# Performance work log

Hardware: AMD Instinct MI355X
Metric: run time of the kernel (lower is better)

## Reference

```python
import jax, jax.numpy as jnp
import numpy as np

N_SPANS = 4096
EMB_DIM = 384
HEADS = 4
DECAY_LAMBDA = 5.0
THRESHOLD = 0.1
NEG_SLOPE = 0.2  # PyG GATConv default leaky_relu slope


def setup_inputs() -> dict:
    key = jax.random.key(0)
    k1, k2, k3, k4, k5, k6 = jax.random.split(key, 6)
    embeddings = jax.random.normal(k1, (N_SPANS, EMB_DIM), dtype=jnp.float32)
    span_positions = jnp.sort(
        jax.random.randint(k2, (N_SPANS, 2), 0, 100000), axis=1
    ).astype(jnp.int64)
    # GATConv params: lin (no bias), per-head attention vectors, output bias
    glorot = 1.0 / np.sqrt(EMB_DIM)
    W = jax.random.normal(k3, (EMB_DIM, HEADS, EMB_DIM), dtype=jnp.float32) * glorot
    att_src = jax.random.normal(k4, (HEADS, EMB_DIM), dtype=jnp.float32) * glorot
    att_dst = jax.random.normal(k5, (HEADS, EMB_DIM), dtype=jnp.float32) * glorot
    bias = jnp.zeros((EMB_DIM,), dtype=jnp.float32)
    return {
        "embeddings": embeddings,
        "span_positions": span_positions,
        "W": W,
        "att_src": att_src,
        "att_dst": att_dst,
        "bias": bias,
    }


def _adjacency_mask(embeddings):
    # A_ij = cos_sim(e_i, e_j) * exp(-|i - j| / lambda); edges where A > 0.1
    n = embeddings.shape[0]
    en = embeddings / jnp.linalg.norm(embeddings, axis=1, keepdims=True)
    cos_sim = en @ en.T  # [N, N]
    idx = jnp.arange(n, dtype=embeddings.dtype)
    decay = jnp.exp(-jnp.abs(idx[None, :] - idx[:, None]) / DECAY_LAMBDA)
    adj = cos_sim * decay
    # diagonal is 1.0 > threshold, so self-loops (required by GATConv) are present
    return adj > THRESHOLD  # symmetric mask: mask[i, j] == edge j -> i


def reference(embeddings, span_positions, W, att_src, att_dst, bias):
    mask = _adjacency_mask(embeddings)  # [N_dst, N_src]
    # GATConv(heads=4, concat=False): project, per-head additive attention
    x = jnp.einsum("nd,dhe->nhe", embeddings, W)  # [N, H, E]
    a_src = jnp.einsum("nhe,he->nh", x, att_src)  # [N, H]
    a_dst = jnp.einsum("nhe,he->nh", x, att_dst)  # [N, H]
    # logits[i, j, h] for edge j -> i
    logits = jax.nn.leaky_relu(a_dst[:, None, :] + a_src[None, :, :], NEG_SLOPE)
    logits = jnp.where(mask[:, :, None], logits, jnp.float32(-jnp.inf))
    alpha = jax.nn.softmax(logits, axis=1)  # softmax over incoming sources j
    out = jnp.einsum("ijh,jhe->ihe", alpha, x)  # [N, H, E]
    out = out.mean(axis=1) + bias  # concat=False -> mean over heads, then bias
    return out
```

## Files before the change

kernel.cpp:

```cpp
#include <hip/hip_runtime.h>
#include <hip/hip_bf16.h>
#include <math.h>

#define N_SPANS 4096
#define EMB 384
#define HEADS 4
#define HE (HEADS * EMB)
#define BAND 11
#define BW (2 * BAND + 1)

typedef short bf16x8 __attribute__((ext_vector_type(8)));
typedef float f32x4 __attribute__((ext_vector_type(4)));

__device__ __forceinline__ unsigned short f2bf(float f) {
    union { float f; unsigned u; } x; x.f = f;
    unsigned r = x.u + 0x7fffu + ((x.u >> 16) & 1u);
    return (unsigned short)(r >> 16);
}
__device__ __forceinline__ float bf2f(unsigned short u) {
    union { unsigned u; float f; } x; x.u = ((unsigned)u) << 16; return x.f;
}

__device__ __forceinline__ float wave_sum(float v) {
    #pragma unroll
    for (int off = 32; off; off >>= 1) v += __shfl_xor(v, off, 64);
    return v;
}
__device__ __forceinline__ float wave_max(float v) {
    #pragma unroll
    for (int off = 32; off; off >>= 1) v = fmaxf(v, __shfl_xor(v, off, 64));
    return v;
}

__device__ __forceinline__ void gl2lds16(const void* g, void* l) {
    __builtin_amdgcn_global_load_lds(
        (const __attribute__((address_space(1))) void*)(uintptr_t)g,
        (__attribute__((address_space(3))) void*)(unsigned)(uintptr_t)l,
        16, 0, 0);
}

__global__ __launch_bounds__(256) void prep(const float* __restrict__ E,
                                            const float* __restrict__ W,
                                            unsigned short* __restrict__ Ebf,
                                            unsigned short* __restrict__ Wt,
                                            float* __restrict__ invn,
                                            float* __restrict__ Dots,
                                            float* __restrict__ attacc) {
    __shared__ float tile[32][33];
    const int b = blockIdx.x;
    const int tid = threadIdx.x;
    if (b < 1024) {
        const int lane = tid & 63, w = tid >> 6;
        const int n = b * 4 + w;
        const float4* er4 = (const float4*)(E + (size_t)n * EMB);
        const int dmax = (n >= N_SPANS - BAND) ? (N_SPANS - 1 - n) : BAND;
        const float4* nb4[BAND];
        #pragma unroll
        for (int d = 1; d <= BAND; ++d) {
            int j = n + d; if (j > N_SPANS - 1) j = N_SPANS - 1;
            nb4[d - 1] = (const float4*)(E + (size_t)j * EMB);
        }
        float acc[12];
        #pragma unroll
        for (int d = 0; d < 12; ++d) acc[d] = 0.f;
        #pragma unroll
        for (int mq = 0; mq < 2; ++mq) {
            const int idx = mq * 64 + lane;
            if (idx < 96) {
                float4 v = er4[idx];
                acc[0] += v.x * v.x + v.y * v.y + v.z * v.z + v.w * v.w;
                ushort4 pb;
                pb.x = f2bf(v.x); pb.y = f2bf(v.y); pb.z = f2bf(v.z); pb.w = f2bf(v.w);
                ((ushort4*)(Ebf + (size_t)n * EMB))[idx] = pb;
                #pragma unroll
                for (int d = 1; d <= BAND; ++d) {
                    float4 u = nb4[d - 1][idx];
                    float dd = v.x * u.x + v.y * u.y + v.z * u.z + v.w * u.w;
                    acc[d] += (d <= dmax) ? dd : 0.f;
                }
            }
        }
        #pragma unroll
        for (int d = 0; d < 12; ++d) acc[d] = wave_sum(acc[d]);
        float dval = 0.f;
        #pragma unroll
        for (int d = 1; d <= BAND; ++d) if (lane == d) dval = acc[d];
        if (lane >= 1 && lane <= BAND) Dots[(size_t)n * 12 + lane] = dval;
        if (lane == 0) invn[n] = 1.0f / sqrtf(acc[0]);
    } else if (b < 1600) {
        const int t = b - 1024;
        const int n0 = (t % 48) * 32;
        const int k0 = (t / 48) * 32;
        const int tx = tid & 31, ty = tid >> 5;
        #pragma unroll
        for (int q = 0; q < 4; ++q)
            tile[ty + q * 8][tx] = W[(k0 + ty + q * 8) * HE + n0 + tx];
        __syncthreads();
        #pragma unroll
        for (int q = 0; q < 4; ++q)
            Wt[(n0 + ty + q * 8) * EMB + k0 + tx] = f2bf(tile[tx][ty + q * 8]);
    } else {
        const int t = b - 1600;
        ((float4*)attacc)[t * 256 + tid] = make_float4(0.f, 0.f, 0.f, 0.f);
    }
}

__global__ __launch_bounds__(256) void gemm_attn(const unsigned short* __restrict__ Ebf,
                                                 const unsigned short* __restrict__ Wt,
                                                 const float* __restrict__ attS,
                                                 const float* __restrict__ attD,
                                                 unsigned short* __restrict__ Xb,
                                                 float* __restrict__ asrc,
                                                 float* __restrict__ adst) {
    __shared__ unsigned short As[128 * 32];
    __shared__ unsigned short Bs[128 * 32];
    const int tid = threadIdx.x;
    const int lane = tid & 63;
    const int wave = tid >> 6;
    const int m0 = blockIdx.y * 128;
    const int n0 = blockIdx.x * 128;
    const int wr = (wave >> 1) * 64;
    const int wc = (wave & 1) * 64;
    const int quad = lane >> 4;
    const int l16 = lane & 15;

    const int schunk = (lane & 3) ^ ((lane >> 3) & 3);
    const char* Ab = (const char*)Ebf + (size_t)(m0 + wave * 32 + (lane >> 2)) * 768 + schunk * 16;
    const char* Bb = (const char*)Wt  + (size_t)(n0 + wave * 32 + (lane >> 2)) * 768 + schunk * 16;
    char* AsB = (char*)As + wave * 32 * 64;
    char* BsB = (char*)Bs + wave * 32 * 64;

    const int rchunk = (quad ^ ((l16 >> 1) & 3)) * 16;

    f32x4 acc[4][4];
    #pragma unroll
    for (int i = 0; i < 4; ++i)
        #pragma unroll
        for (int j = 0; j < 4; ++j) acc[i][j] = 0.f;

    for (int kt = 0; kt < 12; ++kt) {
        const int kb = kt * 64;
        __syncthreads();
        gl2lds16(Ab + kb,            AsB);
        gl2lds16(Ab + kb + 16 * 768, AsB + 16 * 64);
        gl2lds16(Bb + kb,            BsB);
        gl2lds16(Bb + kb + 16 * 768, BsB + 16 * 64);
        __syncthreads();

        bf16x8 af[4], bfr[4];
        #pragma unroll
        for (int t = 0; t < 4; ++t) {
            af[t]  = *(const bf16x8*)((const char*)As + (wr + t * 16 + l16) * 64 + rchunk);
            bfr[t] = *(const bf16x8*)((const char*)Bs + (wc + t * 16 + l16) * 64 + rchunk);
        }
        #pragma unroll
        for (int ti = 0; ti < 4; ++ti)
            #pragma unroll
            for (int tj = 0; tj < 4; ++tj)
                acc[ti][tj] = __builtin_amdgcn_mfma_f32_16x16x32_bf16(
                    af[ti], bfr[tj], acc[ti][tj], 0, 0, 0);
    }

    const int hblk = (n0 + wc) / EMB;
    float aS[4], aD[4];
    #pragma unroll
    for (int tj = 0; tj < 4; ++tj) {
        int col = n0 + wc + tj * 16 + l16;
        aS[tj] = attS[col];
        aD[tj] = attD[col];
    }
    #pragma unroll
    for (int ti = 0; ti < 4; ++ti)
        #pragma unroll
        for (int r = 0; r < 4; ++r) {
            float ps = 0.f, pd = 0.f;
            #pragma unroll
            for (int tj = 0; tj < 4; ++tj) {
                float v = acc[ti][tj][r];
                ps += v * aS[tj];
                pd += v * aD[tj];
            }
            #pragma unroll
            for (int off = 1; off < 16; off <<= 1) {
                ps += __shfl_xor(ps, off, 64);
                pd += __shfl_xor(pd, off, 64);
            }
            if (l16 == 0) {
                int row = m0 + wr + ti * 16 + quad * 4 + r;
                atomicAdd(&asrc[row * HEADS + hblk], ps);
                atomicAdd(&adst[row * HEADS + hblk], pd);
            }
        }

    #pragma unroll
    for (int ti = 0; ti < 4; ++ti)
        #pragma unroll
        for (int tj = 0; tj < 4; ++tj) {
            int col = n0 + wc + tj * 16 + l16;
            #pragma unroll
            for (int r = 0; r < 4; ++r) {
                int row = m0 + wr + ti * 16 + quad * 4 + r;
                Xb[row * HE + col] = f2bf(acc[ti][tj][r]);
            }
        }
}

__global__ __launch_bounds__(256) void band_attn(const float* __restrict__ invn,
                                                 const float* __restrict__ Dots,
                                                 const float* __restrict__ asrc,
                                                 const float* __restrict__ adst,
                                                 const unsigned short* __restrict__ Xb,
                                                 const float* __restrict__ bias,
                                                 float* __restrict__ out) {
    __shared__ float sAl[4][BW][4];
    __shared__ int sList[4][24];
    const int tid = threadIdx.x, lane = tid & 63, w = tid >> 6;
    const int i = blockIdx.x * 4 + w;
    const int jo = lane;
    const int j = i - BAND + jo;
    const bool inb = (jo < BW) && (j >= 0) && (j < N_SPANS);
    const int jc = inb ? j : i;

    float dotv = 0.f;
    if (inb) {
        if (jo < BAND)      dotv = Dots[(size_t)j * 12 + (BAND - jo)];
        else if (jo > BAND) dotv = Dots[(size_t)i * 12 + (jo - BAND)];
    }
    bool flag;
    if (jo == BAND) {
        flag = true;
    } else {
        int dd = jo < BAND ? BAND - jo : jo - BAND;
        float a = ((dotv * invn[i]) * invn[jc]) * expf(-(float)dd * 0.2f);
        flag = inb && (a > 0.1f);
    }

    unsigned long long mbits = __ballot(flag);
    const int cnt = __popcll(mbits);
    const int rank = __popcll(mbits & ((1ull << jo) - 1ull));
    if (flag) sList[w][rank] = jo;

    const float4 ad = ((const float4*)adst)[i];
    const float4 as = inb ? ((const float4*)asrc)[jc] : make_float4(0.f, 0.f, 0.f, 0.f);
    float al[4];
    #pragma unroll
    for (int h = 0; h < 4; ++h) {
        float z = (&ad.x)[h] + (&as.x)[h];
        z = (z >= 0.f) ? z : 0.2f * z;
        float lg = flag ? z : -INFINITY;
        float mx = wave_max(lg);
        float ex = flag ? expf(lg - mx) : 0.f;
        float sm = wave_sum(ex);
        al[h] = ex / sm;
    }
    if (flag) *(float4*)&sAl[w][jo][0] = make_float4(al[0], al[1], al[2], al[3]);

    #pragma unroll
    for (int mq = 0; mq < 2; ++mq) {
        const int e4 = mq * 64 + lane;
        if (e4 < 96) {
            float4 a = make_float4(0.f, 0.f, 0.f, 0.f);
            for (int ii = 0; ii < cnt; ++ii) {
                const int joL = sList[w][ii];
                const int jj = i - BAND + joL;
                const float4 a4 = *(const float4*)&sAl[w][joL][0];
                const ushort4* xr = (const ushort4*)(Xb + (size_t)jj * HE);
                ushort4 h0 = xr[e4], h1 = xr[e4 + 96], h2 = xr[e4 + 192], h3 = xr[e4 + 288];
                a.x += a4.x * bf2f(h0.x) + a4.y * bf2f(h1.x) + a4.z * bf2f(h2.x) + a4.w * bf2f(h3.x);
                a.y += a4.x * bf2f(h0.y) + a4.y * bf2f(h1.y) + a4.z * bf2f(h2.y) + a4.w * bf2f(h3.y);
                a.z += a4.x * bf2f(h0.z) + a4.y * bf2f(h1.z) + a4.z * bf2f(h2.z) + a4.w * bf2f(h3.z);
                a.w += a4.x * bf2f(h0.w) + a4.y * bf2f(h1.w) + a4.z * bf2f(h2.w) + a4.w * bf2f(h3.w);
            }
            const float4 bv = ((const float4*)bias)[e4];
            float4 o;
            o.x = 0.25f * a.x + bv.x;
            o.y = 0.25f * a.y + bv.y;
            o.z = 0.25f * a.z + bv.z;
            o.w = 0.25f * a.w + bv.w;
            ((float4*)(out + (size_t)i * EMB))[e4] = o;
        }
    }
}

extern "C" void kernel_launch(void* const* d_in, const int* in_sizes, int n_in,
                              void* d_out, int out_size, void* d_ws, size_t ws_size,
                              hipStream_t stream) {
    const float* E       = (const float*)d_in[0];
    const float* W       = (const float*)d_in[2];
    const float* att_src = (const float*)d_in[3];
    const float* att_dst = (const float*)d_in[4];
    const float* bias    = (const float*)d_in[5];
    float* out = (float*)d_out;

    char* ws = (char*)d_ws;
    unsigned short* Xb  = (unsigned short*)ws;
    unsigned short* Ebf = (unsigned short*)(ws + 12582912);
    unsigned short* Wt  = (unsigned short*)(ws + 15728640);
    float* invn         = (float*)(ws + 16908288);
    float* asrc         = (float*)(ws + 16924672);
    float* adst         = (float*)(ws + 16990208);
    float* Dots         = (float*)(ws + 17055744);

    prep<<<1632, 256, 0, stream>>>(E, W, Ebf, Wt, invn, Dots, asrc );
    gemm_attn<<<dim3(12, 32), 256, 0, stream>>>(Ebf, Wt, att_src, att_dst, Xb, asrc, adst);
    band_attn<<<1024, 256, 0, stream>>>(invn, Dots, asrc, adst, Xb, bias, out);
}
```

Baseline: 108.1 us.

## Double-buffer GEMM LDS tiles and halve N tile to 64 for more blocks

The projection GEMM now prefetches the next K-slice into a second LDS buffer while computing the current one, removing one barrier per iteration. The N tile shrinks from 128 to 64, doubling the grid from 384 to 768 blocks so the 256 CUs are better filled. The cost is more global reads of the A tile across blocks, fewer MFMAs per LDS load, and twice as many atomic adds for the attention scores.

```diff
diff --git a/kernel.cpp b/kernel.cpp
--- a/kernel.cpp
+++ b/kernel.cpp
@@ -112,60 +112,73 @@
                                                  unsigned short* __restrict__ Xb,
                                                  float* __restrict__ asrc,
                                                  float* __restrict__ adst) {
-    __shared__ unsigned short As[128 * 32];
-    __shared__ unsigned short Bs[128 * 32];
+    __shared__ unsigned short As[2 * 128 * 32];
+    __shared__ unsigned short Bs[2 * 64 * 32];
     const int tid = threadIdx.x;
     const int lane = tid & 63;
     const int wave = tid >> 6;
     const int m0 = blockIdx.y * 128;
-    const int n0 = blockIdx.x * 128;
-    const int wr = (wave >> 1) * 64;
-    const int wc = (wave & 1) * 64;
+    const int n0 = blockIdx.x * 64;
+    const int wrow = (wave >> 1) * 64;
+    const int wcol = (wave & 1) * 32;
     const int quad = lane >> 4;
     const int l16 = lane & 15;
 
     const int schunk = (lane & 3) ^ ((lane >> 3) & 3);
     const char* Ab = (const char*)Ebf + (size_t)(m0 + wave * 32 + (lane >> 2)) * 768 + schunk * 16;
-    const char* Bb = (const char*)Wt  + (size_t)(n0 + wave * 32 + (lane >> 2)) * 768 + schunk * 16;
-    char* AsB = (char*)As + wave * 32 * 64;
-    char* BsB = (char*)Bs + wave * 32 * 64;
+    const char* Bb = (const char*)Wt  + (size_t)(n0 + wave * 16 + (lane >> 2)) * 768 + schunk * 16;
+    char* AsW = (char*)As + wave * 2048;
+    char* BsW = (char*)Bs + wave * 1024;
 
     const int rchunk = (quad ^ ((l16 >> 1) & 3)) * 16;
 
-    f32x4 acc[4][4];
+    f32x4 acc[4][2];
     #pragma unroll
     for (int i = 0; i < 4; ++i)
         #pragma unroll
-        for (int j = 0; j < 4; ++j) acc[i][j] = 0.f;
-
+        for (int j = 0; j < 2; ++j) acc[i][j] = 0.f;
+
+    gl2lds16(Ab,            AsW);
+    gl2lds16(Ab + 16 * 768, AsW + 1024);
+    gl2lds16(Bb,            BsW);
+    __syncthreads();
+
+    int cur = 0;
     for (int kt = 0; kt < 12; ++kt) {
-        const int kb = kt * 64;
-        __syncthreads();
-        gl2lds16(Ab + kb,            AsB);
-        gl2lds16(Ab + kb + 16 * 768, AsB + 16 * 64);
-        gl2lds16(Bb + kb,            BsB);
-        gl2lds16(Bb + kb + 16 * 768, BsB + 16 * 64);
-        __syncthreads();
-
-        bf16x8 af[4], bfr[4];
-        #pragma unroll
-        for (int t = 0; t < 4; ++t) {
-            af[t]  = *(const bf16x8*)((const char*)As + (wr + t * 16 + l16) * 64 + rchunk);
-            bfr[t] = *(const bf16x8*)((const char*)Bs + (wc + t * 16 + l16) * 64 + rchunk);
-        }
+        if (kt < 11) {
+            const int kb = (kt + 1) * 64;
+            const int bufo = (cur ^ 1) * 8192;
+            const int bufoB = (cur ^ 1) * 4096;
+            gl2lds16(Ab + kb,            AsW + bufo);
+            gl2lds16(Ab + kb + 16 * 768, AsW + bufo + 1024);
+            gl2lds16(Bb + kb,            BsW + bufoB);
+        }
+
+        const char* aBase = (const char*)As + cur * 8192;
+        const char* bBase = (const char*)Bs + cur * 4096;
+        bf16x8 af[4], bfr[2];
+        #pragma unroll
+        for (int t = 0; t < 4; ++t)
+            af[t] = *(const bf16x8*)(aBase + (wrow + t * 16 + l16) * 64 + rchunk);
+        #pragma unroll
+        for (int t = 0; t < 2; ++t)
+            bfr[t] = *(const bf16x8*)(bBase + (wcol + t * 16 + l16) * 64 + rchunk);
         #pragma unroll
         for (int ti = 0; ti < 4; ++ti)
             #pragma unroll
-            for (int tj = 0; tj < 4; ++tj)
+            for (int tj = 0; tj < 2; ++tj)
                 acc[ti][tj] = __builtin_amdgcn_mfma_f32_16x16x32_bf16(
                     af[ti], bfr[tj], acc[ti][tj], 0, 0, 0);
-    }
-
-    const int hblk = (n0 + wc) / EMB;
-    float aS[4], aD[4];
-    #pragma unroll
-    for (int tj = 0; tj < 4; ++tj) {
-        int col = n0 + wc + tj * 16 + l16;
+
+        __syncthreads();
+        cur ^= 1;
+    }
+
+    const int hblk = (n0 + wcol) / EMB;
+    float aS[2], aD[2];
+    #pragma unroll
+    for (int tj = 0; tj < 2; ++tj) {
+        int col = n0 + wcol + tj * 16 + l16;
         aS[tj] = attS[col];
         aD[tj] = attD[col];
     }
@@ -175,7 +188,7 @@
         for (int r = 0; r < 4; ++r) {
             float ps = 0.f, pd = 0.f;
             #pragma unroll
-            for (int tj = 0; tj < 4; ++tj) {
+            for (int tj = 0; tj < 2; ++tj) {
                 float v = acc[ti][tj][r];
                 ps += v * aS[tj];
                 pd += v * aD[tj];
@@ -186,7 +199,7 @@
                 pd += __shfl_xor(pd, off, 64);
             }
             if (l16 == 0) {
-                int row = m0 + wr + ti * 16 + quad * 4 + r;
+                int row = m0 + wrow + ti * 16 + quad * 4 + r;
                 atomicAdd(&asrc[row * HEADS + hblk], ps);
                 atomicAdd(&adst[row * HEADS + hblk], pd);
             }
@@ -195,11 +208,11 @@
     #pragma unroll
     for (int ti = 0; ti < 4; ++ti)
         #pragma unroll
-        for (int tj = 0; tj < 4; ++tj) {
-            int col = n0 + wc + tj * 16 + l16;
+        for (int tj = 0; tj < 2; ++tj) {
+            int col = n0 + wcol + tj * 16 + l16;
             #pragma unroll
             for (int r = 0; r < 4; ++r) {
-                int row = m0 + wr + ti * 16 + quad * 4 + r;
+                int row = m0 + wrow + ti * 16 + quad * 4 + r;
                 Xb[row * HE + col] = f2bf(acc[ti][tj][r]);
             }
         }
@@ -302,6 +315,6 @@
     float* Dots         = (float*)(ws + 17055744);
 
     prep<<<1632, 256, 0, stream>>>(E, W, Ebf, Wt, invn, Dots, asrc );
-    gemm_attn<<<dim3(12, 32), 256, 0, stream>>>(Ebf, Wt, att_src, att_dst, Xb, asrc, adst);
+    gemm_attn<<<dim3(24, 32), 256, 0, stream>>>(Ebf, Wt, att_src, att_dst, Xb, asrc, adst);
     band_attn<<<1024, 256, 0, stream>>>(invn, Dots, asrc, adst, Xb, bias, out);
 }
```

Result: slower. 119.1 us (+10.2%).

## Fuse prep and GEMM into one kernel with in-kernel fp32-to-bf16 conversion

Applied to the files above, without the earlier changes.

Merges the prep kernel and the projection GEMM into a single launch. The GEMM now loads fp32 embeddings and W directly, converts them to bf16 in registers and writes them into swizzled LDS, with a register prefetch of the next k-tile. This removes the separate Ebf/Wt staging buffers and the W transpose pass. The attention-score partials are reduced in LDS and written to three per-column-tile partial buffers that band_attn sums, which removes the global atomics and the zero-init pass. In exchange the GEMM does more global fp32 traffic, strided W loads and conversion work per tile, and loses the direct global-to-LDS loads.

```diff
diff --git a/kernel.cpp b/kernel.cpp
--- a/kernel.cpp
+++ b/kernel.cpp
@@ -10,6 +10,7 @@
 #define BW (2 * BAND + 1)
 
 typedef short bf16x8 __attribute__((ext_vector_type(8)));
+typedef short bf16x4 __attribute__((ext_vector_type(4)));
 typedef float f32x4 __attribute__((ext_vector_type(4)));
 
 __device__ __forceinline__ unsigned short f2bf(float f) {
@@ -32,26 +33,158 @@
     return v;
 }
 
-__device__ __forceinline__ void gl2lds16(const void* g, void* l) {
-    __builtin_amdgcn_global_load_lds(
-        (const __attribute__((address_space(1))) void*)(uintptr_t)g,
-        (__attribute__((address_space(3))) void*)(unsigned)(uintptr_t)l,
-        16, 0, 0);
-}
-
-__global__ __launch_bounds__(256) void prep(const float* __restrict__ E,
+__device__ __forceinline__ bf16x4 pack4(float a, float b, float c, float d) {
+    bf16x4 r;
+    r[0] = (short)f2bf(a); r[1] = (short)f2bf(b);
+    r[2] = (short)f2bf(c); r[3] = (short)f2bf(d);
+    return r;
+}
+
+__global__ __launch_bounds__(256) void mega(const float* __restrict__ E,
                                             const float* __restrict__ W,
-                                            unsigned short* __restrict__ Ebf,
-                                            unsigned short* __restrict__ Wt,
+                                            const float* __restrict__ attS,
+                                            const float* __restrict__ attD,
+                                            unsigned short* __restrict__ Xb,
                                             float* __restrict__ invn,
                                             float* __restrict__ Dots,
-                                            float* __restrict__ attacc) {
-    __shared__ float tile[32][33];
+                                            float* __restrict__ asrcP,
+                                            float* __restrict__ adstP) {
+    __shared__ unsigned short As[128 * 32];
+    __shared__ unsigned short Bs[128 * 32];
+    __shared__ float sAS[128], sAD[128];
     const int b = blockIdx.x;
     const int tid = threadIdx.x;
-    if (b < 1024) {
-        const int lane = tid & 63, w = tid >> 6;
-        const int n = b * 4 + w;
+    const int lane = tid & 63, w = tid >> 6;
+
+    if (b < 384) {
+        const int nt = b % 12;
+        const int m0 = (b / 12) * 128;
+        const int n0 = nt * 128;
+        const int wave = w;
+        const int quad = lane >> 4;
+        const int l16 = lane & 15;
+        const int wr = (wave >> 1) * 64;
+        const int wc = (wave & 1) * 64;
+
+        if (tid < 128) { sAS[tid] = 0.f; sAD[tid] = 0.f; }
+
+        const int kAe = (tid & 7) * 4;
+        const int rA = tid >> 3;
+        const int sA = (rA >> 1) & 3;
+        const int cA = kAe >> 3;
+        const unsigned aByte = rA * 64 + ((cA ^ sA) * 16) + (tid & 1) * 8;
+        const float* Ag = E + (size_t)(m0 + rA) * EMB + kAe;
+
+        const int gB = tid & 31, kgB = tid >> 5;
+        const float* Bg = W + (size_t)(kgB * 4) * HE + n0 + gB * 4;
+
+        const int rchunk = (quad ^ ((l16 >> 1) & 3)) * 16;
+
+        f32x4 acc[4][4];
+        #pragma unroll
+        for (int i = 0; i < 4; ++i)
+            #pragma unroll
+            for (int j = 0; j < 4; ++j) acc[i][j] = 0.f;
+
+        float4 fa[4], fb[4];
+        #pragma unroll
+        for (int q = 0; q < 4; ++q)
+            fa[q] = *(const float4*)(Ag + (size_t)q * 32 * EMB);
+        #pragma unroll
+        for (int i = 0; i < 4; ++i)
+            fb[i] = *(const float4*)(Bg + (size_t)i * HE);
+
+        for (int kt = 0; kt < 12; ++kt) {
+            #pragma unroll
+            for (int q = 0; q < 4; ++q)
+                *(bf16x4*)((char*)As + q * 2048 + aByte) =
+                    pack4(fa[q].x, fa[q].y, fa[q].z, fa[q].w);
+            #pragma unroll
+            for (int j = 0; j < 4; ++j) {
+                const int c = gB * 4 + j;
+                const int sB = (c >> 1) & 3;
+                *(bf16x4*)((char*)Bs + c * 64 + (((kgB >> 1) ^ sB) * 16) + (kgB & 1) * 8) =
+                    pack4((&fb[0].x)[j], (&fb[1].x)[j], (&fb[2].x)[j], (&fb[3].x)[j]);
+            }
+            __syncthreads();
+
+            if (kt < 11) {
+                const int ko = (kt + 1) * 32;
+                #pragma unroll
+                for (int q = 0; q < 4; ++q)
+                    fa[q] = *(const float4*)(Ag + (size_t)q * 32 * EMB + ko);
+                #pragma unroll
+                for (int i = 0; i < 4; ++i)
+                    fb[i] = *(const float4*)(Bg + (size_t)(ko + i) * HE);
+            }
+
+            bf16x8 af[4], bfr[4];
+            #pragma unroll
+            for (int t = 0; t < 4; ++t) {
+                af[t]  = *(const bf16x8*)((const char*)As + (wr + t * 16 + l16) * 64 + rchunk);
+                bfr[t] = *(const bf16x8*)((const char*)Bs + (wc + t * 16 + l16) * 64 + rchunk);
+            }
+            #pragma unroll
+            for (int ti = 0; ti < 4; ++ti)
+                #pragma unroll
+                for (int tj = 0; tj < 4; ++tj)
+                    acc[ti][tj] = __builtin_amdgcn_mfma_f32_16x16x32_bf16(
+                        af[ti], bfr[tj], acc[ti][tj], 0, 0, 0);
+
+            __syncthreads();
+        }
+
+        float aS[4], aD[4];
+        #pragma unroll
+        for (int tj = 0; tj < 4; ++tj) {
+            int col = n0 + wc + tj * 16 + l16;
+            aS[tj] = attS[col];
+            aD[tj] = attD[col];
+        }
+        #pragma unroll
+        for (int ti = 0; ti < 4; ++ti)
+            #pragma unroll
+            for (int r = 0; r < 4; ++r) {
+                float ps = 0.f, pd = 0.f;
+                #pragma unroll
+                for (int tj = 0; tj < 4; ++tj) {
+                    float v = acc[ti][tj][r];
+                    ps += v * aS[tj];
+                    pd += v * aD[tj];
+                }
+                #pragma unroll
+                for (int off = 1; off < 16; off <<= 1) {
+                    ps += __shfl_xor(ps, off, 64);
+                    pd += __shfl_xor(pd, off, 64);
+                }
+                if (l16 == 0) {
+                    int lrow = wr + ti * 16 + quad * 4 + r;
+                    atomicAdd(&sAS[lrow], ps);
+                    atomicAdd(&sAD[lrow], pd);
+                }
+            }
+        __syncthreads();
+        {
+            const int p = nt % 3, h = nt / 3;
+            if (tid < 128)
+                asrcP[((size_t)p * N_SPANS + m0 + tid) * HEADS + h] = sAS[tid];
+            else
+                adstP[((size_t)p * N_SPANS + m0 + tid - 128) * HEADS + h] = sAD[tid - 128];
+        }
+
+        #pragma unroll
+        for (int ti = 0; ti < 4; ++ti)
+            #pragma unroll
+            for (int tj = 0; tj < 4; ++tj) {
+                int col = n0 + wc + tj * 16 + l16;
+                #pragma unroll
+                for (int r = 0; r < 4; ++r) {
+                    int row = m0 + wr + ti * 16 + quad * 4 + r;
+                    Xb[row * HE + col] = f2bf(acc[ti][tj][r]);
+                }
+            }
+    } else {
+        const int n = (b - 384) * 4 + w;
         const float4* er4 = (const float4*)(E + (size_t)n * EMB);
         const int dmax = (n >= N_SPANS - BAND) ? (N_SPANS - 1 - n) : BAND;
         const float4* nb4[BAND];
@@ -69,9 +202,6 @@
             if (idx < 96) {
                 float4 v = er4[idx];
                 acc[0] += v.x * v.x + v.y * v.y + v.z * v.z + v.w * v.w;
-                ushort4 pb;
-                pb.x = f2bf(v.x); pb.y = f2bf(v.y); pb.z = f2bf(v.z); pb.w = f2bf(v.w);
-                ((ushort4*)(Ebf + (size_t)n * EMB))[idx] = pb;
                 #pragma unroll
                 for (int d = 1; d <= BAND; ++d) {
                     float4 u = nb4[d - 1][idx];
@@ -87,128 +217,13 @@
         for (int d = 1; d <= BAND; ++d) if (lane == d) dval = acc[d];
         if (lane >= 1 && lane <= BAND) Dots[(size_t)n * 12 + lane] = dval;
         if (lane == 0) invn[n] = 1.0f / sqrtf(acc[0]);
-    } else if (b < 1600) {
-        const int t = b - 1024;
-        const int n0 = (t % 48) * 32;
-        const int k0 = (t / 48) * 32;
-        const int tx = tid & 31, ty = tid >> 5;
-        #pragma unroll
-        for (int q = 0; q < 4; ++q)
-            tile[ty + q * 8][tx] = W[(k0 + ty + q * 8) * HE + n0 + tx];
-        __syncthreads();
-        #pragma unroll
-        for (int q = 0; q < 4; ++q)
-            Wt[(n0 + ty + q * 8) * EMB + k0 + tx] = f2bf(tile[tx][ty + q * 8]);
-    } else {
-        const int t = b - 1600;
-        ((float4*)attacc)[t * 256 + tid] = make_float4(0.f, 0.f, 0.f, 0.f);
-    }
-}
-
-__global__ __launch_bounds__(256) void gemm_attn(const unsigned short* __restrict__ Ebf,
-                                                 const unsigned short* __restrict__ Wt,
-                                                 const float* __restrict__ attS,
-                                                 const float* __restrict__ attD,
-                                                 unsigned short* __restrict__ Xb,
-                                                 float* __restrict__ asrc,
-                                                 float* __restrict__ adst) {
-    __shared__ unsigned short As[128 * 32];
-    __shared__ unsigned short Bs[128 * 32];
-    const int tid = threadIdx.x;
-    const int lane = tid & 63;
-    const int wave = tid >> 6;
-    const int m0 = blockIdx.y * 128;
-    const int n0 = blockIdx.x * 128;
-    const int wr = (wave >> 1) * 64;
-    const int wc = (wave & 1) * 64;
-    const int quad = lane >> 4;
-    const int l16 = lane & 15;
-
-    const int schunk = (lane & 3) ^ ((lane >> 3) & 3);
-    const char* Ab = (const char*)Ebf + (size_t)(m0 + wave * 32 + (lane >> 2)) * 768 + schunk * 16;
-    const char* Bb = (const char*)Wt  + (size_t)(n0 + wave * 32 + (lane >> 2)) * 768 + schunk * 16;
-    char* AsB = (char*)As + wave * 32 * 64;
-    char* BsB = (char*)Bs + wave * 32 * 64;
-
-    const int rchunk = (quad ^ ((l16 >> 1) & 3)) * 16;
-
-    f32x4 acc[4][4];
-    #pragma unroll
-    for (int i = 0; i < 4; ++i)
-        #pragma unroll
-        for (int j = 0; j < 4; ++j) acc[i][j] = 0.f;
-
-    for (int kt = 0; kt < 12; ++kt) {
-        const int kb = kt * 64;
-        __syncthreads();
-        gl2lds16(Ab + kb,            AsB);
-        gl2lds16(Ab + kb + 16 * 768, AsB + 16 * 64);
-        gl2lds16(Bb + kb,            BsB);
-        gl2lds16(Bb + kb + 16 * 768, BsB + 16 * 64);
-        __syncthreads();
-
-        bf16x8 af[4], bfr[4];
-        #pragma unroll
-        for (int t = 0; t < 4; ++t) {
-            af[t]  = *(const bf16x8*)((const char*)As + (wr + t * 16 + l16) * 64 + rchunk);
-            bfr[t] = *(const bf16x8*)((const char*)Bs + (wc + t * 16 + l16) * 64 + rchunk);
-        }
-        #pragma unroll
-        for (int ti = 0; ti < 4; ++ti)
-            #pragma unroll
-            for (int tj = 0; tj < 4; ++tj)
-                acc[ti][tj] = __builtin_amdgcn_mfma_f32_16x16x32_bf16(
-                    af[ti], bfr[tj], acc[ti][tj], 0, 0, 0);
-    }
-
-    const int hblk = (n0 + wc) / EMB;
-    float aS[4], aD[4];
-    #pragma unroll
-    for (int tj = 0; tj < 4; ++tj) {
-        int col = n0 + wc + tj * 16 + l16;
-        aS[tj] = attS[col];
-        aD[tj] = attD[col];
-    }
-    #pragma unroll
-    for (int ti = 0; ti < 4; ++ti)
-        #pragma unroll
-        for (int r = 0; r < 4; ++r) {
-            float ps = 0.f, pd = 0.f;
-            #pragma unroll
-            for (int tj = 0; tj < 4; ++tj) {
-                float v = acc[ti][tj][r];
-                ps += v * aS[tj];
-                pd += v * aD[tj];
-            }
-            #pragma unroll
-            for (int off = 1; off < 16; off <<= 1) {
-                ps += __shfl_xor(ps, off, 64);
-                pd += __shfl_xor(pd, off, 64);
-            }
-            if (l16 == 0) {
-                int row = m0 + wr + ti * 16 + quad * 4 + r;
-                atomicAdd(&asrc[row * HEADS + hblk], ps);
-                atomicAdd(&adst[row * HEADS + hblk], pd);
-            }
-        }
-
-    #pragma unroll
-    for (int ti = 0; ti < 4; ++ti)
-        #pragma unroll
-        for (int tj = 0; tj < 4; ++tj) {
-            int col = n0 + wc + tj * 16 + l16;
-            #pragma unroll
-            for (int r = 0; r < 4; ++r) {
-                int row = m0 + wr + ti * 16 + quad * 4 + r;
-                Xb[row * HE + col] = f2bf(acc[ti][tj][r]);
-            }
-        }
+    }
 }
 
 __global__ __launch_bounds__(256) void band_attn(const float* __restrict__ invn,
                                                  const float* __restrict__ Dots,
-                                                 const float* __restrict__ asrc,
-                                                 const float* __restrict__ adst,
+                                                 const float* __restrict__ asrcP,
+                                                 const float* __restrict__ adstP,
                                                  const unsigned short* __restrict__ Xb,
                                                  const float* __restrict__ bias,
                                                  float* __restrict__ out) {
@@ -240,8 +255,21 @@
     const int rank = __popcll(mbits & ((1ull << jo) - 1ull));
     if (flag) sList[w][rank] = jo;
 
-    const float4 ad = ((const float4*)adst)[i];
-    const float4 as = inb ? ((const float4*)asrc)[jc] : make_float4(0.f, 0.f, 0.f, 0.f);
+    const float4* S4 = (const float4*)asrcP;
+    const float4* D4 = (const float4*)adstP;
+    float4 ad, as;
+    {
+        float4 a0 = D4[i], a1 = D4[N_SPANS + i], a2 = D4[2 * N_SPANS + i];
+        ad = make_float4(a0.x + a1.x + a2.x, a0.y + a1.y + a2.y,
+                         a0.z + a1.z + a2.z, a0.w + a1.w + a2.w);
+        if (inb) {
+            float4 s0 = S4[jc], s1 = S4[N_SPANS + jc], s2 = S4[2 * N_SPANS + jc];
+            as = make_float4(s0.x + s1.x + s2.x, s0.y + s1.y + s2.y,
+                             s0.z + s1.z + s2.z, s0.w + s1.w + s2.w);
+        } else {
+            as = make_float4(0.f, 0.f, 0.f, 0.f);
+        }
+    }
     float al[4];
     #pragma unroll
     for (int h = 0; h < 4; ++h) {
@@ -293,15 +321,12 @@
     float* out = (float*)d_out;
 
     char* ws = (char*)d_ws;
-    unsigned short* Xb  = (unsigned short*)ws;
-    unsigned short* Ebf = (unsigned short*)(ws + 12582912);
-    unsigned short* Wt  = (unsigned short*)(ws + 15728640);
-    float* invn         = (float*)(ws + 16908288);
-    float* asrc         = (float*)(ws + 16924672);
-    float* adst         = (float*)(ws + 16990208);
-    float* Dots         = (float*)(ws + 17055744);
-
-    prep<<<1632, 256, 0, stream>>>(E, W, Ebf, Wt, invn, Dots, asrc );
-    gemm_attn<<<dim3(12, 32), 256, 0, stream>>>(Ebf, Wt, att_src, att_dst, Xb, asrc, adst);
-    band_attn<<<1024, 256, 0, stream>>>(invn, Dots, asrc, adst, Xb, bias, out);
-}
+    unsigned short* Xb = (unsigned short*)ws;
+    float* invn        = (float*)(ws + 12582912);
+    float* Dots        = (float*)(ws + 12599296);
+    float* asrcP       = (float*)(ws + 12795904);
+    float* adstP       = (float*)(ws + 12992512);
+
+    mega<<<1408, 256, 0, stream>>>(E, W, att_src, att_dst, Xb, invn, Dots, asrcP, adstP);
+    band_attn<<<1024, 256, 0, stream>>>(invn, Dots, asrcP, adstP, Xb, bias, out);
+}
```

Result: faster. 99.55 us (-7.9%).
